# Optimization experiments

Hardware: AMD Instinct MI355X
Metric: run time of the kernel (lower is better)

The kernel has to match this reference:

```python
import jax, jax.numpy as jnp
import numpy as np

STEP_NUM = 2
SAMPLE_NUM = 10
SAMPLE_SCOPE = 128
NODE_NUM = 232965
INPUT_DIM = 602
HIDDEN_DIM = 256
OUTPUT_DIM = 41
BATCH = 256


def _forward(ids, feature, edge, weight, sample_W, sample_W2, sample_a, W1, W2):
    # a: softmax over the 3 mixing coefficients (matches softmax_a(sample_a) then mm)
    a = jax.nn.softmax(sample_a, axis=0)[:, 0]  # [3]
    key = jax.random.key(42)
    adj_list = [None] * STEP_NUM
    in_nodes = ids
    for i in range(STEP_NUM):
        layer = STEP_NUM - 1 - i
        nbr = edge[in_nodes]              # [n, S] candidate neighbor ids
        src_f = feature[in_nodes]         # [n, F]
        tgt_f = feature[nbr]              # [n, S, F]
        # GAT-style bilinear attention scores (two heads) + structural weight
        s1 = src_f @ sample_W             # [n, H]
        s2 = src_f @ sample_W2            # [n, H]
        t1 = jnp.einsum('nsf,fh->nsh', tgt_f, sample_W)   # [n, S, H]
        t2 = jnp.einsum('nsf,fh->nsh', tgt_f, sample_W2)  # [n, S, H]
        att1 = jnp.einsum('nh,nsh->ns', s1, t1)
        att2 = jnp.einsum('nh,nsh->ns', s2, t2)
        att3 = weight[in_nodes]           # [n, S]
        att = jax.nn.relu(a[0] * att1 + a[1] * att2 + a[2] * att3) + 1e-9
        # Categorical sampling of SAMPLE_NUM neighbors per node
        key, sk = jax.random.split(key)
        cols = jax.random.categorical(sk, jnp.log(att), shape=(SAMPLE_NUM, in_nodes.shape[0])).T  # [n, K]
        # sub-graph adjacency: row-normalized sampled weights (block-sparse structure)
        w = jnp.take_along_axis(weight[in_nodes], cols, axis=1)  # [n, K]
        adj_list[layer] = w / (w.sum(axis=1, keepdims=True) + 1e-9)
        in_nodes = jnp.take_along_axis(nbr, cols, axis=1).reshape(-1)  # [n*K]
    X = feature[in_nodes]                 # start_feat: deepest frontier features
    Ws = [W1, W2]
    for layer in range(STEP_NUM):
        n = adj_list[layer].shape[0]
        # sparse adjacency matmul == per-row weighted sum over sampled neighbors
        X = jnp.einsum('nk,nkd->nd', adj_list[layer], X.reshape(n, SAMPLE_NUM, -1))
        X = X @ Ws[layer]
        if layer < STEP_NUM - 1:
            X = jax.nn.relu(X)  # dropout is identity in eval
    return X


def setup_inputs() -> dict:
    key = jax.random.key(0)
    ks = jax.random.split(key, 9)
    N1 = NODE_NUM + 1
    return {
        'ids': jax.random.randint(ks[0], (BATCH,), 0, NODE_NUM),
        'feature': jax.random.normal(ks[1], (N1, INPUT_DIM), dtype=jnp.float32),
        'edge': jax.random.randint(ks[2], (N1, SAMPLE_SCOPE), 0, NODE_NUM),
        'weight': jax.random.uniform(ks[3], (N1, SAMPLE_SCOPE), dtype=jnp.float32),
        'sample_W': jax.random.normal(ks[4], (INPUT_DIM, HIDDEN_DIM), dtype=jnp.float32) * 0.05,
        'sample_W2': jax.random.normal(ks[5], (INPUT_DIM, HIDDEN_DIM), dtype=jnp.float32) * 0.05,
        'sample_a': jax.random.normal(ks[6], (3, 1), dtype=jnp.float32),
        'W1': jax.random.normal(ks[7], (INPUT_DIM, HIDDEN_DIM), dtype=jnp.float32) * 0.05,
        'W2': jax.random.normal(ks[8], (HIDDEN_DIM, OUTPUT_DIM), dtype=jnp.float32) * 0.05,
    }


def reference(ids, feature, edge, weight, sample_W, sample_W2, sample_a, W1, W2):
    return _forward(ids, feature, edge, weight, sample_W, sample_W2, sample_a, W1, W2)
```

## Files before the change

kernel.cpp:

```cpp
#include <hip/hip_runtime.h>
#include <cstdint>
#include <cstddef>

#define JAX_PARTITIONABLE 1

#define S_SCOPE 128
#define K_SAMP  10
#define F_DIM   602
#define H_DIM   256
#define O_DIM   41
#define BATCH_N 256

__host__ __device__ __forceinline__ void tf2x32(uint32_t k0, uint32_t k1,
                                                uint32_t x0, uint32_t x1,
                                                uint32_t* o0, uint32_t* o1) {
  uint32_t ks2 = k0 ^ k1 ^ 0x1BD11BDAu;
  x0 += k0; x1 += k1;
#define TF_R(d) { x0 += x1; x1 = (x1 << (d)) | (x1 >> (32 - (d))); x1 ^= x0; }
#define TF_G0 TF_R(13) TF_R(15) TF_R(26) TF_R(6)
#define TF_G1 TF_R(17) TF_R(29) TF_R(16) TF_R(24)
  TF_G0; x0 += k1;  x1 += ks2 + 1u;
  TF_G1; x0 += ks2; x1 += k0  + 2u;
  TF_G0; x0 += k0;  x1 += k1  + 3u;
  TF_G1; x0 += k1;  x1 += ks2 + 4u;
  TF_G0; x0 += ks2; x1 += k0  + 5u;
#undef TF_R
#undef TF_G0
#undef TF_G1
  *o0 = x0; *o1 = x1;
}

__device__ __forceinline__ float jax_gumbel(uint32_t ka, uint32_t kb, uint32_t j, uint32_t M) {
  uint32_t r0, r1, bits;
#if JAX_PARTITIONABLE
  tf2x32(ka, kb, 0u, j, &r0, &r1);
  bits = r0 ^ r1;
#else
  uint32_t half = M >> 1;
  if (j < half) { tf2x32(ka, kb, j, j + half, &r0, &r1); bits = r0; }
  else          { tf2x32(ka, kb, j - half, j, &r0, &r1); bits = r1; }
#endif
  float f = __uint_as_float((bits >> 9) | 0x3f800000u) - 1.0f;
  if (f == 0.0f) f = 1.17549435e-38f;
  return -logf(-logf(f));
}

__device__ __forceinline__ void cand_load(const float* __restrict__ feature,
                                          int nbr, int lane, float2* buf) {
  const float2* fr = (const float2*)(feature + (size_t)nbr * F_DIM);
#pragma unroll
  for (int t = 0; t < 5; ++t) {
    const int p = lane + t * 64;
    buf[t] = (p < F_DIM / 2) ? fr[p] : make_float2(0.f, 0.f);
  }
}

__device__ __forceinline__ void cand_dot(const float2* buf,
                                         const float* g1l, const float* g2l,
                                         int lane, float& d1, float& d2) {
  d1 = 0.f; d2 = 0.f;
#pragma unroll
  for (int t = 0; t < 5; ++t) {
    const int p = lane + t * 64;
    float2 ga, gb;
    if (p < F_DIM / 2) {
      ga = ((const float2*)g1l)[p];
      gb = ((const float2*)g2l)[p];
    } else {
      ga = make_float2(0.f, 0.f);
      gb = make_float2(0.f, 0.f);
    }
    d1 = fmaf(buf[t].x, ga.x, fmaf(buf[t].y, ga.y, d1));
    d2 = fmaf(buf[t].x, gb.x, fmaf(buf[t].y, gb.y, d2));
  }
}

__device__ __forceinline__ void red2(float& d1, float& d2) {
#pragma unroll
  for (int off = 32; off > 0; off >>= 1) {
    d1 += __shfl_xor(d1, off);
    d2 += __shfl_xor(d2, off);
  }
}

template<int FUSE_Y>
__device__ __forceinline__ void att_core(const float* __restrict__ feature,
                                         const float* g1l, const float* g2l,
                                         float* logitl, float* wtl, int* nbrl,
                                         int* coll, float* selw, int* selr,
                                         int nIdx, int n,
                                         float aw0, float aw1, float aw2,
                                         uint32_t ska, uint32_t skb,
                                         float* __restrict__ adj_or_y,
                                         int* __restrict__ out_nodes) {
  constexpr int BLK = 512;
  constexpr int NW = BLK / 64;
  constexpr int NIT = S_SCOPE / NW;
  const int tid = threadIdx.x;
  const int lane = tid & 63;
  const int wave = tid >> 6;

  float2 bufA[5], bufB[5];
  cand_load(feature, nbrl[wave], lane, bufA);
  for (int it = 0; it < NIT; it += 2) {
    const int sA = wave + it * NW;
    const int sB = sA + NW;
    cand_load(feature, nbrl[sB], lane, bufB);
    {
      float d1, d2;
      cand_dot(bufA, g1l, g2l, lane, d1, d2);
      red2(d1, d2);
      if (lane == 0) {
        const float att = fmaxf(aw0 * d1 + aw1 * d2 + aw2 * wtl[sA], 0.0f) + 1e-9f;
        logitl[sA] = logf(att);
      }
    }
    if (it + 2 < NIT) cand_load(feature, nbrl[sB + NW], lane, bufA);
    {
      float d1, d2;
      cand_dot(bufB, g1l, g2l, lane, d1, d2);
      red2(d1, d2);
      if (lane == 0) {
        const float att = fmaxf(aw0 * d1 + aw1 * d2 + aw2 * wtl[sB], 0.0f) + 1e-9f;
        logitl[sB] = logf(att);
      }
    }
  }
  __syncthreads();

  const uint32_t M = (uint32_t)K_SAMP * (uint32_t)n * (uint32_t)S_SCOPE;
  for (int k = wave; k < K_SAMP; k += NW) {
    const uint32_t jbase = ((uint32_t)k * (uint32_t)n + (uint32_t)nIdx) * (uint32_t)S_SCOPE;
    float v0 = logitl[lane]      + jax_gumbel(ska, skb, jbase + (uint32_t)lane,        M);
    float v1 = logitl[lane + 64] + jax_gumbel(ska, skb, jbase + (uint32_t)(lane + 64), M);
    float best = v0; int bidx = lane;
    if (v1 > best) { best = v1; bidx = lane + 64; }
#pragma unroll
    for (int off = 1; off < 64; off <<= 1) {
      const float ov = __shfl_xor(best, off);
      const int oi = __shfl_xor(bidx, off);
      if (ov > best || (ov == best && oi < bidx)) { best = ov; bidx = oi; }
    }
    if (lane == 0) coll[k] = bidx;
  }
  __syncthreads();

  if constexpr (FUSE_Y) {
    if (tid == 0) {
      float w[K_SAMP]; float sum = 0.f;
#pragma unroll
      for (int k = 0; k < K_SAMP; ++k) { w[k] = wtl[coll[k]]; sum += w[k]; }
      const float den = sum + 1e-9f;
#pragma unroll
      for (int k = 0; k < K_SAMP; ++k) {
        selw[k] = w[k] / den;
        selr[k] = nbrl[coll[k]];
      }
    }
    __syncthreads();
    for (int e = tid; e < F_DIM; e += BLK) {
      float acc = 0.f;
#pragma unroll
      for (int k = 0; k < K_SAMP; ++k)
        acc = fmaf(selw[k], feature[(size_t)selr[k] * F_DIM + e], acc);
      adj_or_y[(size_t)nIdx * F_DIM + e] = acc;
    }
  } else {
    if (tid == 0) {
      float w[K_SAMP]; float sum = 0.f;
#pragma unroll
      for (int k = 0; k < K_SAMP; ++k) { w[k] = wtl[coll[k]]; sum += w[k]; }
      const float den = sum + 1e-9f;
#pragma unroll
      for (int k = 0; k < K_SAMP; ++k) {
        adj_or_y[(size_t)nIdx * K_SAMP + k] = w[k] / den;
        out_nodes[nIdx * K_SAMP + k] = nbrl[coll[k]];
      }
    }
  }
}

__global__ void __launch_bounds__(512) k_sgatt0(const float* __restrict__ feature,
                                                const int* __restrict__ edge,
                                                const float* __restrict__ weight,
                                                const float* __restrict__ Wa,
                                                const float* __restrict__ Wb,
                                                const int* __restrict__ nodes,
                                                int n,
                                                const float* __restrict__ sample_a,
                                                uint32_t ska, uint32_t skb,
                                                float* __restrict__ adj,
                                                int* __restrict__ out_nodes) {
  __shared__ __align__(16) float fl[604];
  __shared__ __align__(16) float sl[2][H_DIM];
  __shared__ __align__(16) float g1l[604];
  __shared__ __align__(16) float g2l[604];
  __shared__ float logitl[S_SCOPE];
  __shared__ float wtl[S_SCOPE];
  __shared__ int nbrl[S_SCOPE];
  __shared__ int coll[K_SAMP];

  const int nIdx = blockIdx.x;
  const int tid = threadIdx.x;
  const int node = nodes[nIdx];

  const float a0v = sample_a[0], a1v = sample_a[1], a2v = sample_a[2];
  const float mx = fmaxf(a0v, fmaxf(a1v, a2v));
  const float e0 = expf(a0v - mx), e1 = expf(a1v - mx), e2 = expf(a2v - mx);
  const float inv = 1.0f / (e0 + e1 + e2);
  const float aw0 = e0 * inv, aw1 = e1 * inv, aw2 = e2 * inv;

  {
    const float* src = feature + (size_t)node * F_DIM;
    for (int e = tid; e < 604; e += 512) fl[e] = (e < F_DIM) ? src[e] : 0.f;
    if (tid < S_SCOPE) {
      nbrl[tid] = edge[(size_t)node * S_SCOPE + tid];
      wtl[tid] = weight[(size_t)node * S_SCOPE + tid];
    }
  }
  __syncthreads();

  {
    const int head = tid >> 8;
    const int h = tid & 255;
    const float* __restrict__ W = head ? Wb : Wa;
    float a = 0.f;
    for (int fc = 0; fc < 150; ++fc) {
      const int f = fc * 4;
      const float w0 = W[(size_t)(f + 0) * H_DIM + h];
      const float w1 = W[(size_t)(f + 1) * H_DIM + h];
      const float w2 = W[(size_t)(f + 2) * H_DIM + h];
      const float w3 = W[(size_t)(f + 3) * H_DIM + h];
      const float4 v = *(const float4*)&fl[f];
      a = fmaf(v.x, w0, a); a = fmaf(v.y, w1, a);
      a = fmaf(v.z, w2, a); a = fmaf(v.w, w3, a);
    }
    for (int f = 600; f < 602; ++f) a = fmaf(fl[f], W[(size_t)f * H_DIM + h], a);
    sl[head][h] = a;
  }
  __syncthreads();

  for (int j = 0; j < 3; ++j) {
    const int idx = tid + j * 512;
    if (idx < 2 * F_DIM) {
      const int head = idx >= F_DIM;
      const int f = head ? idx - F_DIM : idx;
      const float* __restrict__ W = head ? Wb : Wa;
      const float4* wr = (const float4*)(W + (size_t)f * H_DIM);
      float b = 0.f;
      for (int hq = 0; hq < H_DIM / 4; ++hq) {
        const float4 w = wr[hq];
        const float4 v = *(const float4*)&sl[head][hq * 4];
        b = fmaf(v.x, w.x, b); b = fmaf(v.y, w.y, b);
        b = fmaf(v.z, w.z, b); b = fmaf(v.w, w.w, b);
      }
      (head ? g2l : g1l)[f] = b;
    }
  }
  __syncthreads();

  att_core<0>(feature, g1l, g2l, logitl, wtl, nbrl, coll, nullptr, nullptr,
              nIdx, n, aw0, aw1, aw2, ska, skb, adj, out_nodes);
}

template<int R>
__global__ void __launch_bounds__(256) k_sg(const float* __restrict__ feature,
                                            const float* __restrict__ Wa,
                                            const float* __restrict__ Wb,
                                            const int* __restrict__ nodes,
                                            float* __restrict__ g1,
                                            float* __restrict__ g2) {
  __shared__ __align__(16) float fl[R][604];
  __shared__ __align__(16) float sl[R][H_DIM];
  const float* __restrict__ W = blockIdx.y ? Wb : Wa;
  float* __restrict__ g = blockIdx.y ? g2 : g1;
  const int r0 = blockIdx.x * R;
  const int tid = threadIdx.x;
  for (int r = 0; r < R; ++r) {
    const float* src = feature + (size_t)nodes[r0 + r] * F_DIM;
    for (int e = tid; e < 604; e += 256) fl[r][e] = (e < F_DIM) ? src[e] : 0.f;
  }
  __syncthreads();

  {
    const int h = tid;
    float a[R];
#pragma unroll
    for (int r = 0; r < R; ++r) a[r] = 0.f;
    for (int fc = 0; fc < 150; ++fc) {
      const int f = fc * 4;
      const float w0 = W[(size_t)(f + 0) * H_DIM + h];
      const float w1 = W[(size_t)(f + 1) * H_DIM + h];
      const float w2 = W[(size_t)(f + 2) * H_DIM + h];
      const float w3 = W[(size_t)(f + 3) * H_DIM + h];
#pragma unroll
      for (int r = 0; r < R; ++r) {
        const float4 v = *(const float4*)&fl[r][f];
        a[r] = fmaf(v.x, w0, a[r]); a[r] = fmaf(v.y, w1, a[r]);
        a[r] = fmaf(v.z, w2, a[r]); a[r] = fmaf(v.w, w3, a[r]);
      }
    }
    for (int f = 600; f < 602; ++f) {
      const float w = W[(size_t)f * H_DIM + h];
#pragma unroll
      for (int r = 0; r < R; ++r) a[r] = fmaf(fl[r][f], w, a[r]);
    }
#pragma unroll
    for (int r = 0; r < R; ++r) sl[r][h] = a[r];
  }
  __syncthreads();

  for (int j = 0; j < 3; ++j) {
    const int f = tid + j * 256;
    if (f < F_DIM) {
      const float4* wr = (const float4*)(W + (size_t)f * H_DIM);
      float b[R];
#pragma unroll
      for (int r = 0; r < R; ++r) b[r] = 0.f;
      for (int hq = 0; hq < H_DIM / 4; ++hq) {
        const float4 w = wr[hq];
#pragma unroll
        for (int r = 0; r < R; ++r) {
          const float4 v = *(const float4*)&sl[r][hq * 4];
          b[r] = fmaf(v.x, w.x, b[r]); b[r] = fmaf(v.y, w.y, b[r]);
          b[r] = fmaf(v.z, w.z, b[r]); b[r] = fmaf(v.w, w.w, b[r]);
        }
      }
#pragma unroll
      for (int r = 0; r < R; ++r)
        g[(size_t)(r0 + r) * F_DIM + f] = b[r];
    }
  }
}

__global__ void __launch_bounds__(512) k_att1(const float* __restrict__ feature,
                                              const int* __restrict__ edge,
                                              const float* __restrict__ weight,
                                              const float* __restrict__ g1,
                                              const float* __restrict__ g2,
                                              const int* __restrict__ nodes,
                                              int n,
                                              const float* __restrict__ sample_a,
                                              uint32_t ska, uint32_t skb,
                                              float* __restrict__ y) {
  __shared__ __align__(16) float g1l[604];
  __shared__ __align__(16) float g2l[604];
  __shared__ float logitl[S_SCOPE];
  __shared__ float wtl[S_SCOPE];
  __shared__ int nbrl[S_SCOPE];
  __shared__ int coll[K_SAMP];
  __shared__ float selw[K_SAMP];
  __shared__ int selr[K_SAMP];

  const int nIdx = blockIdx.x;
  const int tid = threadIdx.x;
  const int node = nodes[nIdx];

  const float a0v = sample_a[0], a1v = sample_a[1], a2v = sample_a[2];
  const float mx = fmaxf(a0v, fmaxf(a1v, a2v));
  const float e0 = expf(a0v - mx), e1 = expf(a1v - mx), e2 = expf(a2v - mx);
  const float inv = 1.0f / (e0 + e1 + e2);
  const float aw0 = e0 * inv, aw1 = e1 * inv, aw2 = e2 * inv;

  for (int e = tid; e < F_DIM; e += 512) {
    g1l[e] = g1[(size_t)nIdx * F_DIM + e];
    g2l[e] = g2[(size_t)nIdx * F_DIM + e];
  }
  if (tid < S_SCOPE) {
    nbrl[tid] = edge[(size_t)node * S_SCOPE + tid];
    wtl[tid] = weight[(size_t)node * S_SCOPE + tid];
  }
  __syncthreads();

  att_core<1>(feature, g1l, g2l, logitl, wtl, nbrl, coll, selw, selr,
              nIdx, n, aw0, aw1, aw2, ska, skb, y, nullptr);
}

__global__ void __launch_bounds__(256) k_out(const float* __restrict__ y,
                                             const float* __restrict__ W1,
                                             const float* __restrict__ adj1,
                                             const float* __restrict__ W2,
                                             float* __restrict__ out) {
  __shared__ __align__(16) float yl[K_SAMP][604];
  __shared__ float zl[H_DIM];
  const int nIdx = blockIdx.x;
  const int r0 = nIdx * K_SAMP;
  const int tid = threadIdx.x;
  for (int r = 0; r < K_SAMP; ++r)
    for (int e = tid; e < 604; e += 256)
      yl[r][e] = (e < F_DIM) ? y[(size_t)(r0 + r) * F_DIM + e] : 0.f;
  __syncthreads();

  const int h = tid;
  float acc[K_SAMP];
#pragma unroll
  for (int r = 0; r < K_SAMP; ++r) acc[r] = 0.f;
  for (int fc = 0; fc < 150; ++fc) {
    const int f = fc * 4;
    const float w0 = W1[(size_t)(f + 0) * H_DIM + h];
    const float w1 = W1[(size_t)(f + 1) * H_DIM + h];
    const float w2 = W1[(size_t)(f + 2) * H_DIM + h];
    const float w3 = W1[(size_t)(f + 3) * H_DIM + h];
#pragma unroll
    for (int r = 0; r < K_SAMP; ++r) {
      const float4 v = *(const float4*)&yl[r][f];
      acc[r] = fmaf(v.x, w0, acc[r]); acc[r] = fmaf(v.y, w1, acc[r]);
      acc[r] = fmaf(v.z, w2, acc[r]); acc[r] = fmaf(v.w, w3, acc[r]);
    }
  }
  for (int f = 600; f < 602; ++f) {
    const float w = W1[(size_t)f * H_DIM + h];
#pragma unroll
    for (int r = 0; r < K_SAMP; ++r) acc[r] = fmaf(yl[r][f], w, acc[r]);
  }

  float z = 0.f;
#pragma unroll
  for (int k = 0; k < K_SAMP; ++k)
    z = fmaf(adj1[(size_t)nIdx * K_SAMP + k], fmaxf(acc[k], 0.f), z);
  zl[h] = z;
  __syncthreads();

  if (tid < O_DIM) {
    float o = 0.f;
    for (int hh = 0; hh < H_DIM; ++hh)
      o = fmaf(zl[hh], W2[(size_t)hh * O_DIM + tid], o);
    out[(size_t)nIdx * O_DIM + tid] = o;
  }
}

extern "C" void kernel_launch(void* const* d_in, const int* in_sizes, int n_in,
                              void* d_out, int out_size, void* d_ws, size_t ws_size,
                              hipStream_t stream) {
  (void)in_sizes; (void)n_in; (void)out_size; (void)ws_size;
  const int*   ids       = (const int*)d_in[0];
  const float* feature   = (const float*)d_in[1];
  const int*   edge      = (const int*)d_in[2];
  const float* weight    = (const float*)d_in[3];
  const float* sample_W  = (const float*)d_in[4];
  const float* sample_W2 = (const float*)d_in[5];
  const float* sample_a  = (const float*)d_in[6];
  const float* W1        = (const float*)d_in[7];
  const float* W2        = (const float*)d_in[8];
  float* out = (float*)d_out;

  const int N1 = BATCH_N;
  const int N2 = BATCH_N * K_SAMP;

  float* ws   = (float*)d_ws;
  float* g1   = ws;
  float* g2   = g1 + (size_t)N2 * F_DIM;
  float* yb   = g2 + (size_t)N2 * F_DIM;
  float* adj1 = yb + (size_t)N2 * F_DIM;
  int*   in1  = (int*)(adj1 + (size_t)N1 * K_SAMP);

  uint32_t k0 = 0u, k1 = 42u;
  uint32_t nk0, nk1, sk0a, sk0b, sk1a, sk1b;
#if JAX_PARTITIONABLE
  {
    tf2x32(k0, k1, 0u, 0u, &nk0, &nk1);
    tf2x32(k0, k1, 0u, 1u, &sk0a, &sk0b);
    tf2x32(nk0, nk1, 0u, 1u, &sk1a, &sk1b);
  }
#else
  {
    uint32_t a0, b0, a1, b1;
    tf2x32(k0, k1, 0u, 2u, &a0, &b0);
    tf2x32(k0, k1, 1u, 3u, &a1, &b1);
    nk0 = a0; nk1 = a1; sk0a = b0; sk0b = b1;
    tf2x32(nk0, nk1, 0u, 2u, &a0, &b0);
    tf2x32(nk0, nk1, 1u, 3u, &a1, &b1);
    sk1a = b0; sk1b = b1;
  }
#endif

  k_sgatt0<<<N1, 512, 0, stream>>>(feature, edge, weight, sample_W, sample_W2,
                                   ids, N1, sample_a, sk0a, sk0b, adj1, in1);
  k_sg<10><<<dim3(N2 / 10, 2), 256, 0, stream>>>(feature, sample_W, sample_W2, in1, g1, g2);
  k_att1<<<N2, 512, 0, stream>>>(feature, edge, weight, g1, g2, in1, N2,
                                 sample_a, sk1a, sk1b, yb);
  k_out<<<N1, 256, 0, stream>>>(yb, W1, adj1, W2, out);
}
```

Before: 397.5 us.

## Split output kernel into parallel hidden matmul and final aggregation; restructure attention loop

The single per-batch-node output kernel (256 blocks each doing 10 rows × 602×256 matmul) is split into k_h, which computes relu(Y·W1) over 640 blocks of 4 rows, and k_final, which does the adjacency-weighted sum and the W2 projection. This raises block-level parallelism for the layer-1 matmul but adds a launch and a round trip of the hidden activations through global memory. The attention candidate loop also drops the software-pipelined double-buffered loads. Instead it processes two candidates per wave at a time with interleaved dot products and reductions.

```diff
diff --git a/kernel.cpp b/kernel.cpp
--- a/kernel.cpp
+++ b/kernel.cpp
@@ -45,85 +45,62 @@
   return -logf(-logf(f));
 }
 
-__device__ __forceinline__ void cand_load(const float* __restrict__ feature,
-                                          int nbr, int lane, float2* buf) {
-  const float2* fr = (const float2*)(feature + (size_t)nbr * F_DIM);
-#pragma unroll
-  for (int t = 0; t < 5; ++t) {
-    const int p = lane + t * 64;
-    buf[t] = (p < F_DIM / 2) ? fr[p] : make_float2(0.f, 0.f);
-  }
-}
-
-__device__ __forceinline__ void cand_dot(const float2* buf,
-                                         const float* g1l, const float* g2l,
-                                         int lane, float& d1, float& d2) {
-  d1 = 0.f; d2 = 0.f;
-#pragma unroll
-  for (int t = 0; t < 5; ++t) {
-    const int p = lane + t * 64;
-    float2 ga, gb;
-    if (p < F_DIM / 2) {
-      ga = ((const float2*)g1l)[p];
-      gb = ((const float2*)g2l)[p];
-    } else {
-      ga = make_float2(0.f, 0.f);
-      gb = make_float2(0.f, 0.f);
-    }
-    d1 = fmaf(buf[t].x, ga.x, fmaf(buf[t].y, ga.y, d1));
-    d2 = fmaf(buf[t].x, gb.x, fmaf(buf[t].y, gb.y, d2));
-  }
-}
-
-__device__ __forceinline__ void red2(float& d1, float& d2) {
-#pragma unroll
-  for (int off = 32; off > 0; off >>= 1) {
-    d1 += __shfl_xor(d1, off);
-    d2 += __shfl_xor(d2, off);
-  }
-}
-
-template<int FUSE_Y>
+template<int FUSE_Y, int BLK>
 __device__ __forceinline__ void att_core(const float* __restrict__ feature,
                                          const float* g1l, const float* g2l,
-                                         float* logitl, float* wtl, int* nbrl,
+                                         float* logitl, const float* wtl,
+                                         const int* nbrl,
                                          int* coll, float* selw, int* selr,
                                          int nIdx, int n,
                                          float aw0, float aw1, float aw2,
                                          uint32_t ska, uint32_t skb,
                                          float* __restrict__ adj_or_y,
                                          int* __restrict__ out_nodes) {
-  constexpr int BLK = 512;
   constexpr int NW = BLK / 64;
-  constexpr int NIT = S_SCOPE / NW;
   const int tid = threadIdx.x;
   const int lane = tid & 63;
   const int wave = tid >> 6;
 
-  float2 bufA[5], bufB[5];
-  cand_load(feature, nbrl[wave], lane, bufA);
-  for (int it = 0; it < NIT; it += 2) {
-    const int sA = wave + it * NW;
+  for (int t16 = 0; t16 < S_SCOPE / (2 * NW); ++t16) {
+    const int sA = wave + t16 * (2 * NW);
     const int sB = sA + NW;
-    cand_load(feature, nbrl[sB], lane, bufB);
-    {
-      float d1, d2;
-      cand_dot(bufA, g1l, g2l, lane, d1, d2);
-      red2(d1, d2);
-      if (lane == 0) {
-        const float att = fmaxf(aw0 * d1 + aw1 * d2 + aw2 * wtl[sA], 0.0f) + 1e-9f;
-        logitl[sA] = logf(att);
-      }
-    }
-    if (it + 2 < NIT) cand_load(feature, nbrl[sB + NW], lane, bufA);
-    {
-      float d1, d2;
-      cand_dot(bufB, g1l, g2l, lane, d1, d2);
-      red2(d1, d2);
-      if (lane == 0) {
-        const float att = fmaxf(aw0 * d1 + aw1 * d2 + aw2 * wtl[sB], 0.0f) + 1e-9f;
-        logitl[sB] = logf(att);
-      }
+    const int nbrA = nbrl[sA];
+    const int nbrB = nbrl[sB];
+    const float wtA = wtl[sA];
+    const float wtB = wtl[sB];
+    const float2* frA = (const float2*)(feature + (size_t)nbrA * F_DIM);
+    const float2* frB = (const float2*)(feature + (size_t)nbrB * F_DIM);
+    float2 vA[5], vB[5], gav[5], gbv[5];
+#pragma unroll
+    for (int t = 0; t < 5; ++t) {
+      const int p = lane + t * 64;
+      if (p < F_DIM / 2) {
+        vA[t] = frA[p]; vB[t] = frB[p];
+        gav[t] = ((const float2*)g1l)[p];
+        gbv[t] = ((const float2*)g2l)[p];
+      } else {
+        vA[t] = make_float2(0.f, 0.f); vB[t] = make_float2(0.f, 0.f);
+        gav[t] = make_float2(0.f, 0.f); gbv[t] = make_float2(0.f, 0.f);
+      }
+    }
+    float d1A = 0.f, d2A = 0.f, d1B = 0.f, d2B = 0.f;
+#pragma unroll
+    for (int t = 0; t < 5; ++t) {
+      d1A = fmaf(vA[t].x, gav[t].x, fmaf(vA[t].y, gav[t].y, d1A));
+      d2A = fmaf(vA[t].x, gbv[t].x, fmaf(vA[t].y, gbv[t].y, d2A));
+      d1B = fmaf(vB[t].x, gav[t].x, fmaf(vB[t].y, gav[t].y, d1B));
+      d2B = fmaf(vB[t].x, gbv[t].x, fmaf(vB[t].y, gbv[t].y, d2B));
+    }
+#pragma unroll
+    for (int off = 32; off > 0; off >>= 1) {
+      d1A += __shfl_xor(d1A, off); d2A += __shfl_xor(d2A, off);
+      d1B += __shfl_xor(d1B, off); d2B += __shfl_xor(d2B, off);
+    }
+    if (lane == 0) {
+      const float attA = fmaxf(aw0 * d1A + aw1 * d2A + aw2 * wtA, 0.0f) + 1e-9f;
+      const float attB = fmaxf(aw0 * d1B + aw1 * d2B + aw2 * wtB, 0.0f) + 1e-9f;
+      logitl[sA] = logf(attA);
+      logitl[sB] = logf(attB);
     }
   }
   __syncthreads();
@@ -259,8 +236,8 @@
   }
   __syncthreads();
 
-  att_core<0>(feature, g1l, g2l, logitl, wtl, nbrl, coll, nullptr, nullptr,
-              nIdx, n, aw0, aw1, aw2, ska, skb, adj, out_nodes);
+  att_core<0, 512>(feature, g1l, g2l, logitl, wtl, nbrl, coll, nullptr, nullptr,
+                   nIdx, n, aw0, aw1, aw2, ska, skb, adj, out_nodes);
 }
 
 template<int R>
@@ -372,29 +349,25 @@
   }
   __syncthreads();
 
-  att_core<1>(feature, g1l, g2l, logitl, wtl, nbrl, coll, selw, selr,
-              nIdx, n, aw0, aw1, aw2, ska, skb, y, nullptr);
-}
-
-__global__ void __launch_bounds__(256) k_out(const float* __restrict__ y,
-                                             const float* __restrict__ W1,
-                                             const float* __restrict__ adj1,
-                                             const float* __restrict__ W2,
-                                             float* __restrict__ out) {
-  __shared__ __align__(16) float yl[K_SAMP][604];
-  __shared__ float zl[H_DIM];
-  const int nIdx = blockIdx.x;
-  const int r0 = nIdx * K_SAMP;
-  const int tid = threadIdx.x;
-  for (int r = 0; r < K_SAMP; ++r)
+  att_core<1, 512>(feature, g1l, g2l, logitl, wtl, nbrl, coll, selw, selr,
+                   nIdx, n, aw0, aw1, aw2, ska, skb, y, nullptr);
+}
+
+#define HROWS 4
+__global__ void __launch_bounds__(256) k_h(const float* __restrict__ y,
+                                           const float* __restrict__ W1,
+                                           float* __restrict__ H) {
+  __shared__ __align__(16) float yl[HROWS][604];
+  const int r0 = blockIdx.x * HROWS;
+  const int tid = threadIdx.x;
+  for (int r = 0; r < HROWS; ++r)
     for (int e = tid; e < 604; e += 256)
       yl[r][e] = (e < F_DIM) ? y[(size_t)(r0 + r) * F_DIM + e] : 0.f;
   __syncthreads();
-
   const int h = tid;
-  float acc[K_SAMP];
-#pragma unroll
-  for (int r = 0; r < K_SAMP; ++r) acc[r] = 0.f;
+  float acc[HROWS];
+#pragma unroll
+  for (int r = 0; r < HROWS; ++r) acc[r] = 0.f;
   for (int fc = 0; fc < 150; ++fc) {
     const int f = fc * 4;
     const float w0 = W1[(size_t)(f + 0) * H_DIM + h];
@@ -402,7 +375,7 @@
     const float w2 = W1[(size_t)(f + 2) * H_DIM + h];
     const float w3 = W1[(size_t)(f + 3) * H_DIM + h];
 #pragma unroll
-    for (int r = 0; r < K_SAMP; ++r) {
+    for (int r = 0; r < HROWS; ++r) {
       const float4 v = *(const float4*)&yl[r][f];
       acc[r] = fmaf(v.x, w0, acc[r]); acc[r] = fmaf(v.y, w1, acc[r]);
       acc[r] = fmaf(v.z, w2, acc[r]); acc[r] = fmaf(v.w, w3, acc[r]);
@@ -411,16 +384,27 @@
   for (int f = 600; f < 602; ++f) {
     const float w = W1[(size_t)f * H_DIM + h];
 #pragma unroll
-    for (int r = 0; r < K_SAMP; ++r) acc[r] = fmaf(yl[r][f], w, acc[r]);
-  }
-
-  float z = 0.f;
+    for (int r = 0; r < HROWS; ++r) acc[r] = fmaf(yl[r][f], w, acc[r]);
+  }
+#pragma unroll
+  for (int r = 0; r < HROWS; ++r)
+    H[(size_t)(r0 + r) * H_DIM + h] = fmaxf(acc[r], 0.f);
+}
+
+__global__ void __launch_bounds__(256) k_final(const float* __restrict__ H,
+                                               const float* __restrict__ adj1,
+                                               const float* __restrict__ W2,
+                                               float* __restrict__ out) {
+  __shared__ float zl[H_DIM];
+  const int nIdx = blockIdx.x;
+  const int tid = threadIdx.x;
+  float acc = 0.f;
 #pragma unroll
   for (int k = 0; k < K_SAMP; ++k)
-    z = fmaf(adj1[(size_t)nIdx * K_SAMP + k], fmaxf(acc[k], 0.f), z);
-  zl[h] = z;
-  __syncthreads();
-
+    acc = fmaf(adj1[(size_t)nIdx * K_SAMP + k],
+               H[(size_t)(nIdx * K_SAMP + k) * H_DIM + tid], acc);
+  zl[tid] = acc;
+  __syncthreads();
   if (tid < O_DIM) {
     float o = 0.f;
     for (int hh = 0; hh < H_DIM; ++hh)
@@ -451,7 +435,8 @@
   float* g1   = ws;
   float* g2   = g1 + (size_t)N2 * F_DIM;
   float* yb   = g2 + (size_t)N2 * F_DIM;
-  float* adj1 = yb + (size_t)N2 * F_DIM;
+  float* Hb   = yb + (size_t)N2 * F_DIM;
+  float* adj1 = Hb + (size_t)N2 * H_DIM;
   int*   in1  = (int*)(adj1 + (size_t)N1 * K_SAMP);
 
   uint32_t k0 = 0u, k1 = 42u;
@@ -479,5 +464,6 @@
   k_sg<10><<<dim3(N2 / 10, 2), 256, 0, stream>>>(feature, sample_W, sample_W2, in1, g1, g2);
   k_att1<<<N2, 512, 0, stream>>>(feature, edge, weight, g1, g2, in1, N2,
                                  sample_a, sk1a, sk1b, yb);
-  k_out<<<N1, 256, 0, stream>>>(yb, W1, adj1, W2, out);
-}
+  k_h<<<N2 / HROWS, 256, 0, stream>>>(yb, W1, Hb);
+  k_final<<<N1, 256, 0, stream>>>(Hb, adj1, W2, out);
+}
```

After: 380.3 us. -4.3%, faster.
